# Optimization experiments

Hardware: AMD Instinct MI355X
Metric: run time of the kernel (lower is better)

Reference implementation:

```python
import jax, jax.numpy as jnp
import numpy as np

B, S, D, H, DI, L = 16, 80, 512, 64, 2048, 6  # batch, seq, d_model, d_lstm(=d_v), d_inner, n_layers
EPS = 1e-6


def _layer_norm(x, g, b):
    m = jnp.mean(x, axis=-1, keepdims=True)
    v = jnp.mean((x - m) ** 2, axis=-1, keepdims=True)
    return (x - m) * jax.lax.rsqrt(v + EPS) * g + b


def _lstm_last(gx, whh):
    # gx: [T, N, 4H] precomputed input-to-gate projections (bias=False LSTM)
    N = gx.shape[1]
    Hh = whh.shape[1]
    init = (jnp.zeros((N, Hh), gx.dtype), jnp.zeros((N, Hh), gx.dtype))

    def step(carry, g_in):
        h, c = carry
        gates = g_in + h @ whh.T  # [N, 4H], torch gate order i,f,g,o
        i, f, g, o = jnp.split(gates, 4, axis=-1)
        c = jax.nn.sigmoid(f) * c + jax.nn.sigmoid(i) * jnp.tanh(g)
        h = jax.nn.sigmoid(o) * jnp.tanh(c)
        return (h, c), None

    (h, _), _ = jax.lax.scan(step, init, gx)
    return h  # [N, H]


def _perm_indices():
    # deterministic janossy permutation: identity with position i swapped to last
    idx = np.arange(S)
    P = np.tile(idx, (S, 1))
    P[idx, idx] = S - 1
    P[idx, S - 1] = idx
    return jnp.asarray(P)  # [S, S]


def _janossy_layer(q, g, b, wih, whh, wfc, P):
    # q: [B, S, D]
    x = _layer_norm(q, g, b)
    # project inputs to gates once, then gather permutations of the projection
    xg = jnp.einsum('bsd,gd->sbg', x, wih)  # [S, B, 4H]
    pg = xg[P]  # [S_i, S_t, B, 4H]: for each output position i, the permuted sequence
    pg = pg.transpose(1, 0, 2, 3).reshape(S, S * B, 4 * H)  # time-major, fold i into batch
    h = _lstm_last(pg, whh)  # [S*B, H]
    h = h.reshape(S, B, H).transpose(1, 0, 2)  # [B, S, H]
    return h @ wfc.T + q  # fc (dropout=identity in eval) + residual


def _ffn(q, g, b, w1, b1, w2, b2):
    x = _layer_norm(q, g, b)
    return jax.nn.relu(x @ w1.T + b1) @ w2.T + b2 + q


def setup_inputs() -> dict:
    key = jax.random.key(0)
    ks = jax.random.split(key, 10)
    n = lambda k, s, sc: jax.random.normal(k, s, jnp.float32) * sc
    return {
        'src_seq': jax.random.normal(ks[0], (B, S, D), jnp.float32),
        'trg_seq': jax.random.normal(ks[1], (B, S, D), jnp.float32),
        'ln1_g': jnp.ones((L, D), jnp.float32),
        'ln1_b': jnp.zeros((L, D), jnp.float32),
        'wih': n(ks[2], (L, 4 * H, D), 0.04),
        'whh': n(ks[3], (L, 4 * H, H), 0.1),
        'wfc': n(ks[4], (L, D, H), 0.05),
        'ln2_g': jnp.ones((L, D), jnp.float32),
        'ln2_b': jnp.zeros((L, D), jnp.float32),
        'w1': n(ks[5], (L, DI, D), 0.03),
        'b1': jnp.zeros((L, DI), jnp.float32),
        'w2': n(ks[6], (L, D, DI), 0.02),
        'b2': jnp.zeros((L, D), jnp.float32),
        'lnf_g': jnp.ones((D,), jnp.float32),
        'lnf_b': jnp.zeros((D,), jnp.float32),
        'wprj': n(ks[7], (1, D), 0.05),
    }


def reference(src_seq, trg_seq, ln1_g, ln1_b, wih, whh, wfc, ln2_g, ln2_b,
              w1, b1, w2, b2, lnf_g, lnf_b, wprj):
    P = _perm_indices()
    x = src_seq
    for l in range(L):  # small fixed layer count
        x = _janossy_layer(x, ln1_g[l], ln1_b[l], wih[l], whh[l], wfc[l], P)
        x = _ffn(x, ln2_g[l], ln2_b[l], w1[l], b1[l], w2[l], b2[l])
    x = _layer_norm(x, lnf_g, lnf_b)
    seq_logit = x @ wprj.T  # [B, S, 1]
    return seq_logit
```

## Files before the change

### kernel.cpp

```cpp
#include <hip/hip_runtime.h>
#include <hip/hip_bf16.h>

#define B_ 16
#define S_ 80
#define D_ 512
#define H_ 64
#define DI_ 2048
#define L_ 6
#define G4H 256
#define NROW (B_ * S_)
#define EPS_ 1e-6f

typedef __attribute__((ext_vector_type(8))) short short8;
typedef __attribute__((ext_vector_type(4))) float f32x4;

__device__ __forceinline__ float sigmoidf_(float x) {
    return __fdividef(1.0f, 1.0f + __expf(-x));
}
__device__ __forceinline__ float tanh_(float x) {
    return __fdividef(2.0f, 1.0f + __expf(-2.0f * x)) - 1.0f;
}
__device__ __forceinline__ short f2bf(float f) {
    __hip_bfloat16 h = __float2bfloat16(f);
    return *reinterpret_cast<short*>(&h);
}

__device__ __forceinline__ void lds_barrier() {
    __asm__ volatile("s_waitcnt lgkmcnt(0)\n\ts_barrier" ::: "memory");
}

__global__ __launch_bounds__(256)
void w2bf_kernel(const float* __restrict__ s, __hip_bfloat16* __restrict__ d, int n4) {
    int i = blockIdx.x * 256 + threadIdx.x;
    if (i < n4) {
        float4 v = reinterpret_cast<const float4*>(s)[i];
        short4 o;
        o.x = f2bf(v.x); o.y = f2bf(v.y); o.z = f2bf(v.z); o.w = f2bf(v.w);
        reinterpret_cast<short4*>(d)[i] = o;
    }
}

__global__ __launch_bounds__(256)
void ln_kernel(const float* __restrict__ x, const float* __restrict__ g,
               const float* __restrict__ b, __hip_bfloat16* __restrict__ out) {
    int row = blockIdx.x;
    int t = threadIdx.x;
    const float* xr = x + (size_t)row * D_;
    float v0 = xr[t], v1 = xr[t + 256];
    __shared__ float ws4[4], qs4[4];
    float s = v0 + v1;
    #pragma unroll
    for (int o = 32; o > 0; o >>= 1) s += __shfl_down(s, o);
    if ((t & 63) == 0) ws4[t >> 6] = s;
    __syncthreads();
    float m = (ws4[0] + ws4[1] + ws4[2] + ws4[3]) * (1.0f / (float)D_);
    float d0 = v0 - m, d1 = v1 - m;
    float q = d0 * d0 + d1 * d1;
    #pragma unroll
    for (int o = 32; o > 0; o >>= 1) q += __shfl_down(q, o);
    if ((t & 63) == 0) qs4[t >> 6] = q;
    __syncthreads();
    float rs = rsqrtf((qs4[0] + qs4[1] + qs4[2] + qs4[3]) * (1.0f / (float)D_) + EPS_);
    __hip_bfloat16* orow = out + (size_t)row * D_;
    orow[t]       = __float2bfloat16(d0 * rs * g[t]       + b[t]);
    orow[t + 256] = __float2bfloat16(d1 * rs * g[t + 256] + b[t + 256]);
}

template<int WITH_BIAS, int WITH_RELU, int WITH_RES, int OUT_MODE>
__global__ __launch_bounds__(256)
void mfma_gemm(const __hip_bfloat16* __restrict__ A, const __hip_bfloat16* __restrict__ W,
               const float* __restrict__ bias, const float* __restrict__ res,
               void* __restrict__ C, int M, int N, int K) {
    const int LDT = 72;
    __shared__ short As[64 * LDT];
    __shared__ short Ws[64 * LDT];

    int tid  = threadIdx.x;
    int wave = tid >> 6, lane = tid & 63;
    int quad = lane >> 4, l16 = lane & 15;
    int m_off = (wave >> 1) * 32, n_off = (wave & 1) * 32;
    int m0 = blockIdx.y * 64, n0 = blockIdx.x * 64;

    int r = tid >> 2, c = tid & 3;
    const short* Ag = reinterpret_cast<const short*>(A);
    const short* Wg = reinterpret_cast<const short*>(W);

    f32x4 acc00 = {0.f,0.f,0.f,0.f}, acc01 = acc00, acc10 = acc00, acc11 = acc00;

    short8 avA[2], avW[2];
    auto load_tile = [&](int k0) {
        const short* arow = &Ag[(size_t)(m0 + r) * K + k0 + c * 16];
        avA[0] = *reinterpret_cast<const short8*>(arow);
        avA[1] = *reinterpret_cast<const short8*>(arow + 8);
        const short* wrow = &Wg[(size_t)(n0 + r) * K + k0 + c * 16];
        avW[0] = *reinterpret_cast<const short8*>(wrow);
        avW[1] = *reinterpret_cast<const short8*>(wrow + 8);
    };

    load_tile(0);
    for (int k0 = 0; k0 < K; k0 += 64) {
        lds_barrier();
        *reinterpret_cast<short8*>(&As[r * LDT + c * 16])     = avA[0];
        *reinterpret_cast<short8*>(&As[r * LDT + c * 16 + 8]) = avA[1];
        *reinterpret_cast<short8*>(&Ws[r * LDT + c * 16])     = avW[0];
        *reinterpret_cast<short8*>(&Ws[r * LDT + c * 16 + 8]) = avW[1];
        lds_barrier();
        if (k0 + 64 < K) load_tile(k0 + 64);

        #pragma unroll
        for (int kc = 0; kc < 2; kc++) {
            short8 a0 = *reinterpret_cast<const short8*>(&As[(m_off + l16) * LDT + kc * 32 + quad * 8]);
            short8 a1 = *reinterpret_cast<const short8*>(&As[(m_off + 16 + l16) * LDT + kc * 32 + quad * 8]);
            short8 b0 = *reinterpret_cast<const short8*>(&Ws[(n_off + l16) * LDT + kc * 32 + quad * 8]);
            short8 b1 = *reinterpret_cast<const short8*>(&Ws[(n_off + 16 + l16) * LDT + kc * 32 + quad * 8]);
            acc00 = __builtin_amdgcn_mfma_f32_16x16x32_bf16(a0, b0, acc00, 0, 0, 0);
            acc01 = __builtin_amdgcn_mfma_f32_16x16x32_bf16(a0, b1, acc01, 0, 0, 0);
            acc10 = __builtin_amdgcn_mfma_f32_16x16x32_bf16(a1, b0, acc10, 0, 0, 0);
            acc11 = __builtin_amdgcn_mfma_f32_16x16x32_bf16(a1, b1, acc11, 0, 0, 0);
        }
    }

    f32x4 accs[2][2] = {{acc00, acc01}, {acc10, acc11}};
    #pragma unroll
    for (int fi = 0; fi < 2; fi++) {
        #pragma unroll
        for (int fj = 0; fj < 2; fj++) {
            int coln = n0 + n_off + fj * 16 + l16;
            float bv = WITH_BIAS ? bias[coln] : 0.0f;
            #pragma unroll
            for (int rr = 0; rr < 4; rr++) {
                int rowm = m0 + m_off + fi * 16 + quad * 4 + rr;
                float v = accs[fi][fj][rr];
                if (WITH_BIAS) v += bv;
                if (WITH_RELU) v = fmaxf(v, 0.0f);
                if (WITH_RES)  v += res[(size_t)rowm * N + coln];
                if (OUT_MODE == 0) {
                    reinterpret_cast<float*>(C)[(size_t)rowm * N + coln] = v;
                } else if (OUT_MODE == 1) {
                    reinterpret_cast<__hip_bfloat16*>(C)[(size_t)rowm * N + coln] = __float2bfloat16(v);
                } else {
                    int b_ = rowm / S_;
                    int s_ = rowm - b_ * S_;
                    int gate = coln >> 6, u = coln & 63;
                    int half = b_ >> 3, slot = b_ & 7;
                    reinterpret_cast<float*>(C)[
                        ((((size_t)(s_ * 2 + half) * 4 + gate) * 64 + u) << 3) + slot] = v;
                }
            }
        }
    }
}

__global__ __launch_bounds__(256)
void lstm_v4_kernel(const float* __restrict__ xg5,
                    const float* __restrict__ whh,
                    __hip_bfloat16* __restrict__ hlast) {
    const int i    = blockIdx.x;
    const int bh   = blockIdx.y;
    const int tid  = threadIdx.x;
    const int wave = tid >> 6, lane = tid & 63;
    const int quad = lane >> 4, l16 = lane & 15;
    const int unit = wave * 16 + l16;

    short8 bfrag[4][2];
    #pragma unroll
    for (int g = 0; g < 4; g++) {
        const float* wr = &whh[(size_t)(g * 64 + unit) * H_];
        #pragma unroll
        for (int kc = 0; kc < 2; kc++) {
            float4 x0 = *(const float4*)(wr + kc * 32 + quad * 8);
            float4 x1 = *(const float4*)(wr + kc * 32 + quad * 8 + 4);
            short8 v;
            v[0] = f2bf(x0.x); v[1] = f2bf(x0.y); v[2] = f2bf(x0.z); v[3] = f2bf(x0.w);
            v[4] = f2bf(x1.x); v[5] = f2bf(x1.y); v[6] = f2bf(x1.z); v[7] = f2bf(x1.w);
            bfrag[g][kc] = v;
        }
    }

    __shared__ __attribute__((aligned(16))) short hsh[2][16][72];
    for (int idx = tid; idx < 2 * 16 * 72; idx += 256)
        reinterpret_cast<short*>(hsh)[idx] = 0;

    float cst[2] = {0.f, 0.f};
    float hvv[2] = {0.f, 0.f};

    size_t xoff[4];
    #pragma unroll
    for (int g = 0; g < 4; g++)
        xoff[g] = ((((size_t)bh * 4 + g) * 64 + unit) << 3) + quad * 2;

    float2 xv[4];
    {
        int s0 = (0 == i) ? (S_ - 1) : 0;
        #pragma unroll
        for (int g = 0; g < 4; g++)
            xv[g] = *reinterpret_cast<const float2*>(&xg5[(size_t)s0 * 4096 + xoff[g]]);
    }

    lds_barrier();

    for (int t = 0; t < S_; t++) {
        const int pb = t & 1;
        short8 af0 = *reinterpret_cast<const short8*>(&hsh[pb][l16][quad * 8]);
        short8 af1 = *reinterpret_cast<const short8*>(&hsh[pb][l16][32 + quad * 8]);

        f32x4 acc[4];
        #pragma unroll
        for (int g = 0; g < 4; g++) {
            f32x4 a = {xv[g].x, xv[g].y, xv[g].x, xv[g].y};
            acc[g] = a;
        }

        if (t + 1 < S_) {
            int tn = t + 1;
            int sn = (tn == i) ? (S_ - 1) : ((tn == S_ - 1) ? i : tn);
            #pragma unroll
            for (int g = 0; g < 4; g++)
                xv[g] = *reinterpret_cast<const float2*>(&xg5[(size_t)sn * 4096 + xoff[g]]);
        }

        #pragma unroll
        for (int g = 0; g < 4; g++) {
            acc[g] = __builtin_amdgcn_mfma_f32_16x16x32_bf16(af0, bfrag[g][0], acc[g], 0, 0, 0);
            acc[g] = __builtin_amdgcn_mfma_f32_16x16x32_bf16(af1, bfrag[g][1], acc[g], 0, 0, 0);
        }

        #pragma unroll
        for (int r = 0; r < 2; r++) {
            float ig = sigmoidf_(acc[0][r]);
            float fg = sigmoidf_(acc[1][r]);
            float gg = tanh_(acc[2][r]);
            float og = sigmoidf_(acc[3][r]);
            float cc = fg * cst[r] + ig * gg;
            cst[r] = cc;
            float h = og * tanh_(cc);
            hvv[r] = h;
            hsh[pb ^ 1][quad * 4 + r][unit] = f2bf(h);
        }
        lds_barrier();
    }

    #pragma unroll
    for (int r = 0; r < 2; r++) {
        int b = bh * 8 + quad * 2 + r;
        hlast[((size_t)b * S_ + i) * H_ + unit] = __float2bfloat16(hvv[r]);
    }
}

__global__ __launch_bounds__(256)
void final_kernel(const float* __restrict__ x, const float* __restrict__ g,
                  const float* __restrict__ b, const float* __restrict__ wprj,
                  float* __restrict__ out) {
    int row = blockIdx.x;
    int t = threadIdx.x;
    const float* xr = x + (size_t)row * D_;
    float v0 = xr[t], v1 = xr[t + 256];
    __shared__ float red[256];
    red[t] = v0 + v1;
    __syncthreads();
    for (int o = 128; o > 0; o >>= 1) { if (t < o) red[t] += red[t + o]; __syncthreads(); }
    float m = red[0] * (1.0f / (float)D_);
    __syncthreads();
    float d0 = v0 - m, d1 = v1 - m;
    red[t] = d0 * d0 + d1 * d1;
    __syncthreads();
    for (int o = 128; o > 0; o >>= 1) { if (t < o) red[t] += red[t + o]; __syncthreads(); }
    float rs = rsqrtf(red[0] * (1.0f / (float)D_) + EPS_);
    __syncthreads();
    float y0 = (d0 * rs * g[t] + b[t]) * wprj[t];
    float y1 = (d1 * rs * g[t + 256] + b[t + 256]) * wprj[t + 256];
    red[t] = y0 + y1;
    __syncthreads();
    for (int o = 128; o > 0; o >>= 1) { if (t < o) red[t] += red[t + o]; __syncthreads(); }
    if (t == 0) out[row] = red[0];
}

extern "C" void kernel_launch(void* const* d_in, const int* in_sizes, int n_in,
                              void* d_out, int out_size, void* d_ws, size_t ws_size,
                              hipStream_t stream) {
    const float* src   = (const float*)d_in[0];
    const float* ln1_g = (const float*)d_in[2];
    const float* ln1_b = (const float*)d_in[3];
    const float* wih   = (const float*)d_in[4];
    const float* whh   = (const float*)d_in[5];
    const float* wfc   = (const float*)d_in[6];
    const float* ln2_g = (const float*)d_in[7];
    const float* ln2_b = (const float*)d_in[8];
    const float* w1    = (const float*)d_in[9];
    const float* b1    = (const float*)d_in[10];
    const float* w2    = (const float*)d_in[11];
    const float* b2    = (const float*)d_in[12];
    const float* lnf_g = (const float*)d_in[13];
    const float* lnf_b = (const float*)d_in[14];
    const float* wprj  = (const float*)d_in[15];
    float* out = (float*)d_out;

    char* ws = (char*)d_ws;
    float* xcur = (float*)ws;                       ws += (size_t)NROW * D_  * 4;
    __hip_bfloat16* lnb = (__hip_bfloat16*)ws;      ws += (size_t)NROW * D_  * 2;
    float* xg5  = (float*)ws;                       ws += (size_t)S_ * 4096  * 4;
    __hip_bfloat16* hb  = (__hip_bfloat16*)ws;      ws += (size_t)NROW * H_  * 2;
    __hip_bfloat16* f1  = (__hip_bfloat16*)ws;      ws += (size_t)NROW * DI_ * 2;
    __hip_bfloat16* wihb = (__hip_bfloat16*)ws;     ws += (size_t)L_ * G4H * D_ * 2;
    __hip_bfloat16* wfcb = (__hip_bfloat16*)ws;     ws += (size_t)L_ * D_ * H_ * 2;
    __hip_bfloat16* w1b  = (__hip_bfloat16*)ws;     ws += (size_t)L_ * DI_ * D_ * 2;
    __hip_bfloat16* w2b  = (__hip_bfloat16*)ws;     ws += (size_t)L_ * D_ * DI_ * 2;

    {
        int n4;
        n4 = L_ * G4H * D_ / 4;
        w2bf_kernel<<<(n4 + 255) / 256, 256, 0, stream>>>(wih, wihb, n4);
        n4 = L_ * D_ * H_ / 4;
        w2bf_kernel<<<(n4 + 255) / 256, 256, 0, stream>>>(wfc, wfcb, n4);
        n4 = L_ * DI_ * D_ / 4;
        w2bf_kernel<<<(n4 + 255) / 256, 256, 0, stream>>>(w1, w1b, n4);
        n4 = L_ * D_ * DI_ / 4;
        w2bf_kernel<<<(n4 + 255) / 256, 256, 0, stream>>>(w2, w2b, n4);
    }

    hipMemcpyAsync(xcur, src, (size_t)NROW * D_ * sizeof(float),
                   hipMemcpyDeviceToDevice, stream);

    for (int l = 0; l < L_; l++) {
        ln_kernel<<<NROW, 256, 0, stream>>>(xcur, ln1_g + (size_t)l * D_,
                                            ln1_b + (size_t)l * D_, lnb);
        mfma_gemm<0, 0, 0, 2><<<dim3(G4H / 64, NROW / 64), 256, 0, stream>>>(
            lnb, wihb + (size_t)l * G4H * D_, nullptr, nullptr, xg5, NROW, G4H, D_);
        lstm_v4_kernel<<<dim3(S_, 2), 256, 0, stream>>>(
            xg5, whh + (size_t)l * G4H * H_, hb);
        mfma_gemm<0, 0, 1, 0><<<dim3(D_ / 64, NROW / 64), 256, 0, stream>>>(
            hb, wfcb + (size_t)l * D_ * H_, nullptr, xcur, xcur, NROW, D_, H_);
        ln_kernel<<<NROW, 256, 0, stream>>>(xcur, ln2_g + (size_t)l * D_,
                                            ln2_b + (size_t)l * D_, lnb);
        mfma_gemm<1, 1, 0, 1><<<dim3(DI_ / 64, NROW / 64), 256, 0, stream>>>(
            lnb, w1b + (size_t)l * DI_ * D_, b1 + (size_t)l * DI_, nullptr, f1, NROW, DI_, D_);
        mfma_gemm<1, 0, 1, 0><<<dim3(D_ / 64, NROW / 64), 256, 0, stream>>>(
            f1, w2b + (size_t)l * D_ * DI_, b2 + (size_t)l * D_, xcur, xcur, NROW, D_, DI_);
    }
    final_kernel<<<NROW, 256, 0, stream>>>(xcur, lnf_g, lnf_b, wprj, out);
}
```

Before: 711.7 us.

## Restructure LSTM recurrence so each wave owns two batches without block barriers

The LSTM kernel now has each wave process its own pair of batch rows, holding the full Whh matrix as bf16 MFMA fragments in registers. The fragments are pre-packed once by a new kernel. The per-step block-wide barrier goes away, since each wave exchanges gates and hidden state through its own private LDS region with a swizzled layout. The input-gate projection is prefetched two steps ahead, and the gemm output layout changes to match. In exchange, each wave issues 16x more MFMAs per step with N-dimension waste, since only 2 of 16 columns are useful, and register pressure is high.

```diff
diff --git a/kernel.cpp b/kernel.cpp
--- a/kernel.cpp
+++ b/kernel.cpp
@@ -38,6 +38,19 @@
         o.x = f2bf(v.x); o.y = f2bf(v.y); o.z = f2bf(v.z); o.w = f2bf(v.w);
         reinterpret_cast<short4*>(d)[i] = o;
     }
+}
+
+__global__ __launch_bounds__(256)
+void whh_frag_kernel(const float* __restrict__ whh, __hip_bfloat16* __restrict__ wfb) {
+    int idx = blockIdx.x * 256 + threadIdx.x;
+    int j    = idx & 7;
+    int lane = (idx >> 3) & 63;
+    int kc   = (idx >> 9) & 1;
+    int t16  = (idx >> 10) & 15;
+    int l    = idx >> 14;
+    int row = 16 * t16 + (lane & 15);
+    int col = kc * 32 + ((lane >> 4) & 3) * 8 + j;
+    wfb[idx] = __float2bfloat16(whh[((size_t)l * G4H + row) * H_ + col]);
 }
 
 __global__ __launch_bounds__(256)
@@ -142,109 +155,110 @@
                     int b_ = rowm / S_;
                     int s_ = rowm - b_ * S_;
                     int gate = coln >> 6, u = coln & 63;
-                    int half = b_ >> 3, slot = b_ & 7;
+                    int bp = b_ >> 1, b2 = b_ & 1;
                     reinterpret_cast<float*>(C)[
-                        ((((size_t)(s_ * 2 + half) * 4 + gate) * 64 + u) << 3) + slot] = v;
+                        (((size_t)s_ * 4 + gate) * 8 + bp) * 128 + (u << 1) + b2] = v;
                 }
             }
         }
     }
 }
 
-__global__ __launch_bounds__(256)
-void lstm_v4_kernel(const float* __restrict__ xg5,
-                    const float* __restrict__ whh,
+__global__ __launch_bounds__(256, 1)
+void lstm_v5_kernel(const float* __restrict__ xg7,
+                    const __hip_bfloat16* __restrict__ wfb,
                     __hip_bfloat16* __restrict__ hlast) {
     const int i    = blockIdx.x;
-    const int bh   = blockIdx.y;
     const int tid  = threadIdx.x;
     const int wave = tid >> 6, lane = tid & 63;
     const int quad = lane >> 4, l16 = lane & 15;
-    const int unit = wave * 16 + l16;
-
-    short8 bfrag[4][2];
-    #pragma unroll
-    for (int g = 0; g < 4; g++) {
-        const float* wr = &whh[(size_t)(g * 64 + unit) * H_];
-        #pragma unroll
-        for (int kc = 0; kc < 2; kc++) {
-            float4 x0 = *(const float4*)(wr + kc * 32 + quad * 8);
-            float4 x1 = *(const float4*)(wr + kc * 32 + quad * 8 + 4);
-            short8 v;
-            v[0] = f2bf(x0.x); v[1] = f2bf(x0.y); v[2] = f2bf(x0.z); v[3] = f2bf(x0.w);
-            v[4] = f2bf(x1.x); v[5] = f2bf(x1.y); v[6] = f2bf(x1.z); v[7] = f2bf(x1.w);
-            bfrag[g][kc] = v;
+    const int bp   = blockIdx.y * 4 + wave;
+
+    __shared__ __attribute__((aligned(16))) short hsh[4][16][72];
+    __shared__ __attribute__((aligned(16))) float gbf[4][64 * 2 * 4];
+
+    {
+        int* hp = reinterpret_cast<int*>(&hsh[wave][0][0]);
+        #pragma unroll
+        for (int k = 0; k < 9; k++) hp[lane + 64 * k] = 0;
+    }
+
+    short8 wf[16][2];
+    {
+        const short* ws = reinterpret_cast<const short*>(wfb);
+        #pragma unroll
+        for (int t16 = 0; t16 < 16; t16++)
+            #pragma unroll
+            for (int kc = 0; kc < 2; kc++)
+                wf[t16][kc] = *reinterpret_cast<const short8*>(
+                    &ws[(((t16 * 2 + kc) * 64) + lane) * 8]);
+    }
+
+    char* gb = reinterpret_cast<char*>(&gbf[wave][0]);
+    const int swr = ((lane >> 2) & 3) << 4;
+
+    float cst0 = 0.f, cst1 = 0.f, h0 = 0.f, h1 = 0.f;
+
+    float2 xva[4], xvb[4];
+    auto xload = [&](float2 (&xv)[4], int t) {
+        int s = (t == i) ? (S_ - 1) : ((t == S_ - 1) ? i : t);
+        const float* xb = xg7 + (size_t)s * 4096 + (size_t)bp * 128 + lane * 2;
+        #pragma unroll
+        for (int g = 0; g < 4; g++)
+            xv[g] = *reinterpret_cast<const float2*>(xb + g * 1024);
+    };
+    xload(xva, 0);
+    xload(xvb, 1);
+    __asm__ volatile("s_waitcnt lgkmcnt(0)" ::: "memory");
+
+    const f32x4 zacc = {0.f, 0.f, 0.f, 0.f};
+
+    auto step = [&](int t, float2 (&xc)[4]) {
+        short8 bf0 = *reinterpret_cast<const short8*>(&hsh[wave][l16][quad * 8]);
+        short8 bf1 = *reinterpret_cast<const short8*>(&hsh[wave][l16][32 + quad * 8]);
+
+        f32x4 acc[16];
+        #pragma unroll
+        for (int t16 = 0; t16 < 16; t16++)
+            acc[t16] = __builtin_amdgcn_mfma_f32_16x16x32_bf16(wf[t16][0], bf0, zacc, 0, 0, 0);
+        #pragma unroll
+        for (int t16 = 0; t16 < 16; t16++)
+            acc[t16] = __builtin_amdgcn_mfma_f32_16x16x32_bf16(wf[t16][1], bf1, acc[t16], 0, 0, 0);
+
+        if (l16 < 2) {
+            #pragma unroll
+            for (int mm = 0; mm < 4; mm++)
+                #pragma unroll
+                for (int r = 0; r < 4; r++) {
+                    int u = 16 * mm + 4 * quad + r;
+                    f32x4 v = {acc[mm][r], acc[4 + mm][r], acc[8 + mm][r], acc[12 + mm][r]};
+                    *reinterpret_cast<f32x4*>(gb + ((u * 32 + l16 * 16) ^ (quad << 4))) = v;
+                }
         }
-    }
-
-    __shared__ __attribute__((aligned(16))) short hsh[2][16][72];
-    for (int idx = tid; idx < 2 * 16 * 72; idx += 256)
-        reinterpret_cast<short*>(hsh)[idx] = 0;
-
-    float cst[2] = {0.f, 0.f};
-    float hvv[2] = {0.f, 0.f};
-
-    size_t xoff[4];
-    #pragma unroll
-    for (int g = 0; g < 4; g++)
-        xoff[g] = ((((size_t)bh * 4 + g) * 64 + unit) << 3) + quad * 2;
-
-    float2 xv[4];
-    {
-        int s0 = (0 == i) ? (S_ - 1) : 0;
-        #pragma unroll
-        for (int g = 0; g < 4; g++)
-            xv[g] = *reinterpret_cast<const float2*>(&xg5[(size_t)s0 * 4096 + xoff[g]]);
-    }
-
-    lds_barrier();
-
-    for (int t = 0; t < S_; t++) {
-        const int pb = t & 1;
-        short8 af0 = *reinterpret_cast<const short8*>(&hsh[pb][l16][quad * 8]);
-        short8 af1 = *reinterpret_cast<const short8*>(&hsh[pb][l16][32 + quad * 8]);
-
-        f32x4 acc[4];
-        #pragma unroll
-        for (int g = 0; g < 4; g++) {
-            f32x4 a = {xv[g].x, xv[g].y, xv[g].x, xv[g].y};
-            acc[g] = a;
-        }
-
-        if (t + 1 < S_) {
-            int tn = t + 1;
-            int sn = (tn == i) ? (S_ - 1) : ((tn == S_ - 1) ? i : tn);
-            #pragma unroll
-            for (int g = 0; g < 4; g++)
-                xv[g] = *reinterpret_cast<const float2*>(&xg5[(size_t)sn * 4096 + xoff[g]]);
-        }
-
-        #pragma unroll
-        for (int g = 0; g < 4; g++) {
-            acc[g] = __builtin_amdgcn_mfma_f32_16x16x32_bf16(af0, bfrag[g][0], acc[g], 0, 0, 0);
-            acc[g] = __builtin_amdgcn_mfma_f32_16x16x32_bf16(af1, bfrag[g][1], acc[g], 0, 0, 0);
-        }
-
-        #pragma unroll
-        for (int r = 0; r < 2; r++) {
-            float ig = sigmoidf_(acc[0][r]);
-            float fg = sigmoidf_(acc[1][r]);
-            float gg = tanh_(acc[2][r]);
-            float og = sigmoidf_(acc[3][r]);
-            float cc = fg * cst[r] + ig * gg;
-            cst[r] = cc;
-            float h = og * tanh_(cc);
-            hvv[r] = h;
-            hsh[pb ^ 1][quad * 4 + r][unit] = f2bf(h);
-        }
-        lds_barrier();
-    }
-
-    #pragma unroll
-    for (int r = 0; r < 2; r++) {
-        int b = bh * 8 + quad * 2 + r;
-        hlast[((size_t)b * S_ + i) * H_ + unit] = __float2bfloat16(hvv[r]);
-    }
+        __asm__ volatile("s_waitcnt lgkmcnt(0)" ::: "memory");
+
+        f32x4 ga = *reinterpret_cast<const f32x4*>(gb + ((lane * 32)      ^ swr));
+        f32x4 gc = *reinterpret_cast<const f32x4*>(gb + ((lane * 32 + 16) ^ swr));
+
+        float i0 = ga[0] + xc[0].x, f0 = ga[1] + xc[1].x, g0 = ga[2] + xc[2].x, o0 = ga[3] + xc[3].x;
+        float i1 = gc[0] + xc[0].y, f1 = gc[1] + xc[1].y, g1 = gc[2] + xc[2].y, o1 = gc[3] + xc[3].y;
+
+        if (t + 2 < S_) xload(xc, t + 2);
+
+        cst0 = sigmoidf_(f0) * cst0 + sigmoidf_(i0) * tanh_(g0);
+        cst1 = sigmoidf_(f1) * cst1 + sigmoidf_(i1) * tanh_(g1);
+        h0 = sigmoidf_(o0) * tanh_(cst0);
+        h1 = sigmoidf_(o1) * tanh_(cst1);
+
+        hsh[wave][0][lane] = f2bf(h0);
+        hsh[wave][1][lane] = f2bf(h1);
+        __asm__ volatile("s_waitcnt lgkmcnt(0)" ::: "memory");
+    };
+
+    for (int t = 0; t < S_; t += 2) { step(t, xva); step(t + 1, xvb); }
+
+    hlast[((size_t)(bp * 2 + 0) * S_ + i) * H_ + lane] = __float2bfloat16(h0);
+    hlast[((size_t)(bp * 2 + 1) * S_ + i) * H_ + lane] = __float2bfloat16(h1);
 }
 
 __global__ __launch_bounds__(256)
@@ -298,13 +312,14 @@
     char* ws = (char*)d_ws;
     float* xcur = (float*)ws;                       ws += (size_t)NROW * D_  * 4;
     __hip_bfloat16* lnb = (__hip_bfloat16*)ws;      ws += (size_t)NROW * D_  * 2;
-    float* xg5  = (float*)ws;                       ws += (size_t)S_ * 4096  * 4;
+    float* xg7  = (float*)ws;                       ws += (size_t)S_ * 4096  * 4;
     __hip_bfloat16* hb  = (__hip_bfloat16*)ws;      ws += (size_t)NROW * H_  * 2;
     __hip_bfloat16* f1  = (__hip_bfloat16*)ws;      ws += (size_t)NROW * DI_ * 2;
     __hip_bfloat16* wihb = (__hip_bfloat16*)ws;     ws += (size_t)L_ * G4H * D_ * 2;
     __hip_bfloat16* wfcb = (__hip_bfloat16*)ws;     ws += (size_t)L_ * D_ * H_ * 2;
     __hip_bfloat16* w1b  = (__hip_bfloat16*)ws;     ws += (size_t)L_ * DI_ * D_ * 2;
     __hip_bfloat16* w2b  = (__hip_bfloat16*)ws;     ws += (size_t)L_ * D_ * DI_ * 2;
+    __hip_bfloat16* whf  = (__hip_bfloat16*)ws;     ws += (size_t)L_ * 16384 * 2;
 
     {
         int n4;
@@ -316,6 +331,7 @@
         w2bf_kernel<<<(n4 + 255) / 256, 256, 0, stream>>>(w1, w1b, n4);
         n4 = L_ * D_ * DI_ / 4;
         w2bf_kernel<<<(n4 + 255) / 256, 256, 0, stream>>>(w2, w2b, n4);
+        whh_frag_kernel<<<(L_ * 16384) / 256, 256, 0, stream>>>(whh, whf);
     }
 
     hipMemcpyAsync(xcur, src, (size_t)NROW * D_ * sizeof(float),
@@ -325,9 +341,9 @@
         ln_kernel<<<NROW, 256, 0, stream>>>(xcur, ln1_g + (size_t)l * D_,
                                             ln1_b + (size_t)l * D_, lnb);
         mfma_gemm<0, 0, 0, 2><<<dim3(G4H / 64, NROW / 64), 256, 0, stream>>>(
-            lnb, wihb + (size_t)l * G4H * D_, nullptr, nullptr, xg5, NROW, G4H, D_);
-        lstm_v4_kernel<<<dim3(S_, 2), 256, 0, stream>>>(
-            xg5, whh + (size_t)l * G4H * H_, hb);
+            lnb, wihb + (size_t)l * G4H * D_, nullptr, nullptr, xg7, NROW, G4H, D_);
+        lstm_v5_kernel<<<dim3(S_, 2), 256, 0, stream>>>(
+            xg7, whf + (size_t)l * 16384, hb);
         mfma_gemm<0, 0, 1, 0><<<dim3(D_ / 64, NROW / 64), 256, 0, stream>>>(
             hb, wfcb + (size_t)l * D_ * H_, nullptr, xcur, xcur, NROW, D_, H_);
         ln_kernel<<<NROW, 256, 0, stream>>>(xcur, ln2_g + (size_t)l * D_,
```

Result: slower. 944.6 us (+32.7%).

## Process both batch halves per LSTM block to interleave two independent recurrences

Applied to the files above, without the earlier changes.

The LSTM recurrence kernel now has each block handle both 8-batch halves for its permutation index, instead of splitting them across two blocks. Two independent MFMA chains and gate computations run per timestep, which gives instruction-level parallelism to hide MFMA and transcendental latency on the serial critical path. The cost is half as many blocks (80 instead of 160 on a GPU with many CUs), more registers, and more work per step.

```diff
diff --git a/kernel.cpp b/kernel.cpp
--- a/kernel.cpp
+++ b/kernel.cpp
@@ -152,11 +152,10 @@
 }
 
 __global__ __launch_bounds__(256)
-void lstm_v4_kernel(const float* __restrict__ xg5,
+void lstm_v6_kernel(const float* __restrict__ xg5,
                     const float* __restrict__ whh,
                     __hip_bfloat16* __restrict__ hlast) {
     const int i    = blockIdx.x;
-    const int bh   = blockIdx.y;
     const int tid  = threadIdx.x;
     const int wave = tid >> 6, lane = tid & 63;
     const int quad = lane >> 4, l16 = lane & 15;
@@ -177,73 +176,92 @@
         }
     }
 
-    __shared__ __attribute__((aligned(16))) short hsh[2][16][72];
-    for (int idx = tid; idx < 2 * 16 * 72; idx += 256)
+    __shared__ __attribute__((aligned(16))) short hsh[2][2][16][72];
+    for (int idx = tid; idx < 2 * 2 * 16 * 72; idx += 256)
         reinterpret_cast<short*>(hsh)[idx] = 0;
 
-    float cst[2] = {0.f, 0.f};
-    float hvv[2] = {0.f, 0.f};
-
-    size_t xoff[4];
-    #pragma unroll
-    for (int g = 0; g < 4; g++)
-        xoff[g] = ((((size_t)bh * 4 + g) * 64 + unit) << 3) + quad * 2;
-
-    float2 xv[4];
-    {
-        int s0 = (0 == i) ? (S_ - 1) : 0;
-        #pragma unroll
-        for (int g = 0; g < 4; g++)
-            xv[g] = *reinterpret_cast<const float2*>(&xg5[(size_t)s0 * 4096 + xoff[g]]);
-    }
+    float cstA[2] = {0.f, 0.f}, cstB[2] = {0.f, 0.f};
+    float hvA[2]  = {0.f, 0.f}, hvB[2]  = {0.f, 0.f};
+
+    size_t xoffA[4], xoffB[4];
+    #pragma unroll
+    for (int g = 0; g < 4; g++) {
+        xoffA[g] = (((size_t)(0 * 4 + g) * 64 + unit) << 3) + quad * 2;
+        xoffB[g] = (((size_t)(1 * 4 + g) * 64 + unit) << 3) + quad * 2;
+    }
+
+    float2 xvA[4], xvB[4];
+    auto xload = [&](int t) {
+        int s = (t == i) ? (S_ - 1) : ((t == S_ - 1) ? i : t);
+        const float* base = xg5 + (size_t)s * 4096;
+        #pragma unroll
+        for (int g = 0; g < 4; g++) {
+            xvA[g] = *reinterpret_cast<const float2*>(base + xoffA[g]);
+            xvB[g] = *reinterpret_cast<const float2*>(base + xoffB[g]);
+        }
+    };
+    xload(0);
 
     lds_barrier();
 
     for (int t = 0; t < S_; t++) {
         const int pb = t & 1;
-        short8 af0 = *reinterpret_cast<const short8*>(&hsh[pb][l16][quad * 8]);
-        short8 af1 = *reinterpret_cast<const short8*>(&hsh[pb][l16][32 + quad * 8]);
-
-        f32x4 acc[4];
+        short8 a0A = *reinterpret_cast<const short8*>(&hsh[0][pb][l16][quad * 8]);
+        short8 a1A = *reinterpret_cast<const short8*>(&hsh[0][pb][l16][32 + quad * 8]);
+        short8 a0B = *reinterpret_cast<const short8*>(&hsh[1][pb][l16][quad * 8]);
+        short8 a1B = *reinterpret_cast<const short8*>(&hsh[1][pb][l16][32 + quad * 8]);
+
+        f32x4 accA[4], accB[4];
         #pragma unroll
         for (int g = 0; g < 4; g++) {
-            f32x4 a = {xv[g].x, xv[g].y, xv[g].x, xv[g].y};
-            acc[g] = a;
-        }
-
-        if (t + 1 < S_) {
-            int tn = t + 1;
-            int sn = (tn == i) ? (S_ - 1) : ((tn == S_ - 1) ? i : tn);
-            #pragma unroll
-            for (int g = 0; g < 4; g++)
-                xv[g] = *reinterpret_cast<const float2*>(&xg5[(size_t)sn * 4096 + xoff[g]]);
-        }
+            accA[g] = f32x4{xvA[g].x, xvA[g].y, 0.f, 0.f};
+            accB[g] = f32x4{xvB[g].x, xvB[g].y, 0.f, 0.f};
+        }
+
+        if (t + 1 < S_) xload(t + 1);
 
         #pragma unroll
         for (int g = 0; g < 4; g++) {
-            acc[g] = __builtin_amdgcn_mfma_f32_16x16x32_bf16(af0, bfrag[g][0], acc[g], 0, 0, 0);
-            acc[g] = __builtin_amdgcn_mfma_f32_16x16x32_bf16(af1, bfrag[g][1], acc[g], 0, 0, 0);
+            accA[g] = __builtin_amdgcn_mfma_f32_16x16x32_bf16(a0A, bfrag[g][0], accA[g], 0, 0, 0);
+            accA[g] = __builtin_amdgcn_mfma_f32_16x16x32_bf16(a1A, bfrag[g][1], accA[g], 0, 0, 0);
+            accB[g] = __builtin_amdgcn_mfma_f32_16x16x32_bf16(a0B, bfrag[g][0], accB[g], 0, 0, 0);
+            accB[g] = __builtin_amdgcn_mfma_f32_16x16x32_bf16(a1B, bfrag[g][1], accB[g], 0, 0, 0);
         }
 
         #pragma unroll
         for (int r = 0; r < 2; r++) {
-            float ig = sigmoidf_(acc[0][r]);
-            float fg = sigmoidf_(acc[1][r]);
-            float gg = tanh_(acc[2][r]);
-            float og = sigmoidf_(acc[3][r]);
-            float cc = fg * cst[r] + ig * gg;
-            cst[r] = cc;
-            float h = og * tanh_(cc);
-            hvv[r] = h;
-            hsh[pb ^ 1][quad * 4 + r][unit] = f2bf(h);
+            {
+                float ig = sigmoidf_(accA[0][r]);
+                float fg = sigmoidf_(accA[1][r]);
+                float gg = tanh_(accA[2][r]);
+                float og = sigmoidf_(accA[3][r]);
+                float cc = fg * cstA[r] + ig * gg;
+                cstA[r] = cc;
+                float h = og * tanh_(cc);
+                hvA[r] = h;
+                hsh[0][pb ^ 1][quad * 4 + r][unit] = f2bf(h);
+            }
+            {
+                float ig = sigmoidf_(accB[0][r]);
+                float fg = sigmoidf_(accB[1][r]);
+                float gg = tanh_(accB[2][r]);
+                float og = sigmoidf_(accB[3][r]);
+                float cc = fg * cstB[r] + ig * gg;
+                cstB[r] = cc;
+                float h = og * tanh_(cc);
+                hvB[r] = h;
+                hsh[1][pb ^ 1][quad * 4 + r][unit] = f2bf(h);
+            }
         }
         lds_barrier();
     }
 
     #pragma unroll
     for (int r = 0; r < 2; r++) {
-        int b = bh * 8 + quad * 2 + r;
-        hlast[((size_t)b * S_ + i) * H_ + unit] = __float2bfloat16(hvv[r]);
+        int bA = quad * 2 + r;
+        int bB = 8 + quad * 2 + r;
+        hlast[((size_t)bA * S_ + i) * H_ + unit] = __float2bfloat16(hvA[r]);
+        hlast[((size_t)bB * S_ + i) * H_ + unit] = __float2bfloat16(hvB[r]);
     }
 }
 
@@ -326,7 +344,7 @@
                                             ln1_b + (size_t)l * D_, lnb);
         mfma_gemm<0, 0, 0, 2><<<dim3(G4H / 64, NROW / 64), 256, 0, stream>>>(
             lnb, wihb + (size_t)l * G4H * D_, nullptr, nullptr, xg5, NROW, G4H, D_);
-        lstm_v4_kernel<<<dim3(S_, 2), 256, 0, stream>>>(
+        lstm_v6_kernel<<<dim3(S_), 256, 0, stream>>>(
             xg5, whh + (size_t)l * G4H * H_, hb);
         mfma_gemm<0, 0, 1, 0><<<dim3(D_ / 64, NROW / 64), 256, 0, stream>>>(
             hb, wfcb + (size_t)l * D_ * H_, nullptr, xcur, xcur, NROW, D_, H_);
```

After: 950.8 us. +33.6%, slower.

## Prefetch LSTM gate inputs into an LDS ring via async global-to-LDS loads

Applied to the files above, without the earlier changes.

The LSTM recurrence kernel now stages each timestep's precomputed input gate projections into a 4-deep shared-memory ring using global_load_lds, issued three steps ahead. Explicit vmcnt waits precede each barrier. Previously each step fetched its inputs straight from global memory into registers only one step ahead. The aim is to hide global memory latency on the serial recurrence path, at the cost of 32KB more LDS, hand-tuned wait counts, and the accumulator upper lanes now initialised to zero instead of duplicated values.

```diff
diff --git a/kernel.cpp b/kernel.cpp
--- a/kernel.cpp
+++ b/kernel.cpp
@@ -27,6 +27,12 @@
 
 __device__ __forceinline__ void lds_barrier() {
     __asm__ volatile("s_waitcnt lgkmcnt(0)\n\ts_barrier" ::: "memory");
+}
+
+__device__ __forceinline__ void gll16(const float* g, float* l) {
+    __builtin_amdgcn_global_load_lds(
+        (const __attribute__((address_space(1))) unsigned int*)g,
+        (__attribute__((address_space(3))) unsigned int*)l, 16, 0, 0);
 }
 
 __global__ __launch_bounds__(256)
@@ -151,8 +157,8 @@
     }
 }
 
-__global__ __launch_bounds__(256)
-void lstm_v4_kernel(const float* __restrict__ xg5,
+__global__ __launch_bounds__(256, 1)
+void lstm_v7_kernel(const float* __restrict__ xg5,
                     const float* __restrict__ whh,
                     __hip_bfloat16* __restrict__ hlast) {
     const int i    = blockIdx.x;
@@ -178,46 +184,47 @@
     }
 
     __shared__ __attribute__((aligned(16))) short hsh[2][16][72];
+    __shared__ __attribute__((aligned(16))) float xring[4][2048];
+
     for (int idx = tid; idx < 2 * 16 * 72; idx += 256)
         reinterpret_cast<short*>(hsh)[idx] = 0;
 
+    auto stage = [&](int t) {
+        int s = (t == i) ? (S_ - 1) : ((t == S_ - 1) ? i : t);
+        const float* gsrc = xg5 + ((size_t)s * 2 + bh) * 2048;
+        float* lbase = &xring[t & 3][0];
+        #pragma unroll
+        for (int j = 0; j < 2; j++) {
+            int off = (j * 4 + wave) * 256;
+            gll16(gsrc + off + lane * 4, lbase + off);
+        }
+    };
+
     float cst[2] = {0.f, 0.f};
     float hvv[2] = {0.f, 0.f};
 
-    size_t xoff[4];
-    #pragma unroll
-    for (int g = 0; g < 4; g++)
-        xoff[g] = ((((size_t)bh * 4 + g) * 64 + unit) << 3) + quad * 2;
-
-    float2 xv[4];
-    {
-        int s0 = (0 == i) ? (S_ - 1) : 0;
-        #pragma unroll
-        for (int g = 0; g < 4; g++)
-            xv[g] = *reinterpret_cast<const float2*>(&xg5[(size_t)s0 * 4096 + xoff[g]]);
-    }
-
+    stage(0); stage(1); stage(2);
+    __asm__ volatile("s_waitcnt vmcnt(4)" ::: "memory");
     lds_barrier();
 
     for (int t = 0; t < S_; t++) {
         const int pb = t & 1;
+        if (t + 3 < S_) stage(t + 3);
+
         short8 af0 = *reinterpret_cast<const short8*>(&hsh[pb][l16][quad * 8]);
         short8 af1 = *reinterpret_cast<const short8*>(&hsh[pb][l16][32 + quad * 8]);
 
+        const float* xb = &xring[t & 3][(unit << 3) + quad * 2];
+        float2 xv0 = *reinterpret_cast<const float2*>(xb);
+        float2 xv1 = *reinterpret_cast<const float2*>(xb + 512);
+        float2 xv2 = *reinterpret_cast<const float2*>(xb + 1024);
+        float2 xv3 = *reinterpret_cast<const float2*>(xb + 1536);
+
         f32x4 acc[4];
-        #pragma unroll
-        for (int g = 0; g < 4; g++) {
-            f32x4 a = {xv[g].x, xv[g].y, xv[g].x, xv[g].y};
-            acc[g] = a;
-        }
-
-        if (t + 1 < S_) {
-            int tn = t + 1;
-            int sn = (tn == i) ? (S_ - 1) : ((tn == S_ - 1) ? i : tn);
-            #pragma unroll
-            for (int g = 0; g < 4; g++)
-                xv[g] = *reinterpret_cast<const float2*>(&xg5[(size_t)sn * 4096 + xoff[g]]);
-        }
+        acc[0] = f32x4{xv0.x, xv0.y, 0.f, 0.f};
+        acc[1] = f32x4{xv1.x, xv1.y, 0.f, 0.f};
+        acc[2] = f32x4{xv2.x, xv2.y, 0.f, 0.f};
+        acc[3] = f32x4{xv3.x, xv3.y, 0.f, 0.f};
 
         #pragma unroll
         for (int g = 0; g < 4; g++) {
@@ -237,6 +244,10 @@
             hvv[r] = h;
             hsh[pb ^ 1][quad * 4 + r][unit] = f2bf(h);
         }
+
+        if (t < 77)       { __asm__ volatile("s_waitcnt vmcnt(4)" ::: "memory"); }
+        else if (t == 77) { __asm__ volatile("s_waitcnt vmcnt(2)" ::: "memory"); }
+        else if (t == 78) { __asm__ volatile("s_waitcnt vmcnt(0)" ::: "memory"); }
         lds_barrier();
     }
 
@@ -326,7 +337,7 @@
                                             ln1_b + (size_t)l * D_, lnb);
         mfma_gemm<0, 0, 0, 2><<<dim3(G4H / 64, NROW / 64), 256, 0, stream>>>(
             lnb, wihb + (size_t)l * G4H * D_, nullptr, nullptr, xg5, NROW, G4H, D_);
-        lstm_v4_kernel<<<dim3(S_, 2), 256, 0, stream>>>(
+        lstm_v7_kernel<<<dim3(S_, 2), 256, 0, stream>>>(
             xg5, whh + (size_t)l * G4H * H_, hb);
         mfma_gemm<0, 0, 1, 0><<<dim3(D_ / 64, NROW / 64), 256, 0, stream>>>(
             hb, wfcb + (size_t)l * D_ * H_, nullptr, xcur, xcur, NROW, D_, H_);
```

Result: slower. 826.7 us (+16.2%).
